# Performance work log

Measured on AMD Instinct MI355X. Metric: run time of the kernel, lower is better.

The kernel has to match this reference:

```python
import jax, jax.numpy as jnp
import numpy as np

NUM_TOURS = 200   # fixed segment count (original: tour_index.max()+1)
EPS = 1e-5        # torch InstanceNorm1d default eps


def setup_inputs() -> dict:
    key = jax.random.key(0)
    ks = jax.random.split(key, 9)
    B, P, D = 64, 2000, 128
    embeddings = jax.random.normal(ks[0], (B, P + 1, D), jnp.float32)
    tour_index = jax.random.randint(ks[1], (B, P), 0, NUM_TOURS, dtype=jnp.int32)
    # tour_combiner: Linear(2D -> D); feedforward: Linear(D -> D); stored as (in, out)
    W1 = jax.random.normal(ks[2], (2 * D, D), jnp.float32) / np.sqrt(2 * D)
    b1 = jax.random.normal(ks[3], (D,), jnp.float32) * 0.01
    W2 = jax.random.normal(ks[4], (D, D), jnp.float32) / np.sqrt(D)
    b2 = jax.random.normal(ks[5], (D,), jnp.float32) * 0.01
    # InstanceNorm1d affine params (per channel)
    gamma = 1.0 + 0.1 * jax.random.normal(ks[6], (D,), jnp.float32)
    beta = 0.1 * jax.random.normal(ks[7], (D,), jnp.float32)
    return {
        "batch_size": B, "num_customers": P,
        "tour_index": tour_index, "embeddings": embeddings,
        "W1": W1, "b1": b1, "W2": W2, "b2": b2,
        "gamma": gamma, "beta": beta,
    }


def reference(batch_size, num_customers, tour_index, embeddings, W1, b1, W2, b2, gamma, beta):
    B, P = batch_size, num_customers
    D = embeddings.shape[-1]
    cust = embeddings[:, 1:]                                  # (B, P, D)
    # tour-level segment sum (scatter_add over tour ids, per batch)
    flat_idx = (tour_index + jnp.arange(B, dtype=tour_index.dtype)[:, None] * NUM_TOURS).reshape(-1)
    tour_emb = jax.ops.segment_sum(cust.reshape(B * P, D), flat_idx,
                                   num_segments=B * NUM_TOURS).reshape(B, NUM_TOURS, D)
    # gather tour embedding back to each customer
    cust_tour = jnp.take_along_axis(tour_emb, tour_index[:, :, None], axis=1)  # (B, P, D)
    # concat -> linear -> relu -> linear
    combined = jnp.concatenate([cust, cust_tour], axis=-1)    # (B, P, 2D)
    h = jax.nn.relu(combined @ W1 + b1)
    h = h @ W2 + b2
    # residual + instance norm over the customer axis, per channel
    added = cust + h
    mean = jnp.mean(added, axis=1, keepdims=True)
    var = jnp.var(added, axis=1, keepdims=True)
    normed = (added - mean) * jax.lax.rsqrt(var + EPS) * gamma + beta
    return jnp.concatenate([embeddings[:, :1], normed], axis=1)
```

## Files before the change

kernel.cpp:

```cpp
#include <hip/hip_runtime.h>
#include <stdint.h>

typedef unsigned short u16;
typedef __attribute__((ext_vector_type(8))) short short8;
typedef __attribute__((ext_vector_type(4))) float floatx4;

constexpr int B_ = 64, P_ = 2000, D_ = 128, T_ = 200;

__device__ __forceinline__ u16 f2bf(float f) {
  union { float f; uint32_t u; } v; v.f = f;
  return (u16)((v.u + 0x7fffu + ((v.u >> 16) & 1u)) >> 16);
}

__global__ void k_zero(float* __restrict__ p, int n) {
  int i = blockIdx.x * 256 + threadIdx.x;
  if (i < n) p[i] = 0.f;
}

__global__ void k_prep_w(const float* __restrict__ W1, const float* __restrict__ W2,
                         u16* __restrict__ w1f, u16* __restrict__ w2f) {
  int tid = blockIdx.x * 256 + threadIdx.x;
  if (tid >= 6144) return;
  const float* W = (tid < 4096) ? W1 : W2;
  u16* dst = (tid < 4096) ? w1f : w2f;
  int fid = (tid < 4096) ? tid : tid - 4096;
  int lane = fid & 63;
  int nt = (fid >> 6) & 7;
  int ks = fid >> 9;
  int quad = lane >> 4, c = lane & 15;
  int k0 = ks * 32 + quad * 8;
#pragma unroll
  for (int j = 0; j < 8; ++j)
    dst[(size_t)fid * 8 + j] = f2bf(W[(k0 + j) * D_ + nt * 16 + c]);
}

__global__ __launch_bounds__(256) void k_bin(const int* __restrict__ tidx,
                                             int* __restrict__ list,
                                             int* __restrict__ goff,
                                             int* __restrict__ gcnt) {
  __shared__ int tix[P_];
  __shared__ int cnt[256], scan[256], cur[256];
  const int b = blockIdx.x, tid = threadIdx.x;
  cnt[tid] = 0;
  for (int i = tid; i < P_; i += 256) tix[i] = tidx[b * P_ + i];
  __syncthreads();
  for (int i = tid; i < P_; i += 256) atomicAdd(&cnt[tix[i]], 1);
  __syncthreads();
  scan[tid] = cnt[tid];
  __syncthreads();
  for (int s = 1; s < 256; s <<= 1) {
    int v = (tid >= s) ? scan[tid - s] : 0;
    __syncthreads();
    scan[tid] += v;
    __syncthreads();
  }
  int excl = scan[tid] - cnt[tid];
  if (tid < T_) {
    goff[b * T_ + tid] = excl;
    gcnt[b * T_ + tid] = cnt[tid];
  }
  cur[tid] = excl;
  __syncthreads();
  for (int i = tid; i < P_; i += 256) {
    int slot = atomicAdd(&cur[tix[i]], 1);
    list[b * P_ + slot] = i;
  }
}

__global__ __launch_bounds__(256) void k_gather(const float* __restrict__ emb,
                                                const int* __restrict__ list,
                                                const int* __restrict__ goff,
                                                const int* __restrict__ gcnt,
                                                u16* __restrict__ tourb) {
  const int tid = threadIdx.x;
  const int lane = tid & 63, wv = tid >> 6;
  const int seg = blockIdx.x * 4 + wv;
  const int b = seg / T_;
  const int off = goff[seg], cn = gcnt[seg];
  const int* lstb = list + b * P_;
  const float* eb = emb + ((size_t)(b * 2001 + 1)) * D_ + lane * 2;
  float sx = 0.f, sy = 0.f;
  for (int i = 0; i < cn; i += 8) {
    int pr[8];
#pragma unroll
    for (int j = 0; j < 8; ++j)
      if (i + j < cn) pr[j] = lstb[off + i + j];
    float2 v[8];
#pragma unroll
    for (int j = 0; j < 8; ++j)
      if (i + j < cn) v[j] = *(const float2*)(eb + (size_t)pr[j] * D_);
#pragma unroll
    for (int j = 0; j < 8; ++j)
      if (i + j < cn) { sx += v[j].x; sy += v[j].y; }
  }
  uint32_t pk = (uint32_t)f2bf(sx) | ((uint32_t)f2bf(sy) << 16);
  ((uint32_t*)(tourb + (size_t)seg * D_))[lane] = pk;
}

__global__ __launch_bounds__(256) void k_mlp(
    const int* __restrict__ tidx, const float* __restrict__ emb,
    const u16* __restrict__ tourb,
    const u16* __restrict__ w1f, const u16* __restrict__ w2f,
    const float* __restrict__ b1, const float* __restrict__ b2,
    float* __restrict__ out) {
  __shared__ u16 hbuf[128 * 136];
  const int tid = threadIdx.x;
  const int w = tid >> 6, lane = tid & 63, quad = lane >> 4, c = lane & 15;
  const int base = blockIdx.x * 128;
  const int r0 = w * 32;

  const float* arow[2];
  const u16* trow[2];
#pragma unroll
  for (int mt = 0; mt < 2; ++mt) {
    int m = base + r0 + mt * 16 + c;
    int b = m / P_, p = m - b * P_;
    arow[mt] = emb + ((size_t)(b * 2001 + 1 + p)) * D_;
    int t = tidx[m];
    trow[mt] = tourb + ((size_t)(b * T_ + t)) * D_;
  }
  float bias1[8], bias2[8];
#pragma unroll
  for (int nt = 0; nt < 8; ++nt) {
    bias1[nt] = b1[nt * 16 + c];
    bias2[nt] = b2[nt * 16 + c];
  }

  floatx4 acc[2][8];
#pragma unroll
  for (int mt = 0; mt < 2; ++mt)
#pragma unroll
    for (int nt = 0; nt < 8; ++nt) acc[mt][nt] = (floatx4)0.f;

#pragma unroll
  for (int ks = 0; ks < 8; ++ks) {
    short8 a[2];
#pragma unroll
    for (int mt = 0; mt < 2; ++mt) {
      if (ks < 4) {
        const float* src = arow[mt] + ks * 32 + quad * 8;
        floatx4 x0 = *(const floatx4*)src;
        floatx4 x1 = *(const floatx4*)(src + 4);
#pragma unroll
        for (int j = 0; j < 4; ++j) {
          a[mt][j]     = (short)f2bf(x0[j]);
          a[mt][4 + j] = (short)f2bf(x1[j]);
        }
      } else {
        a[mt] = *(const short8*)(trow[mt] + (ks - 4) * 32 + quad * 8);
      }
    }
#pragma unroll
    for (int nt = 0; nt < 8; ++nt) {
      short8 bf = *(const short8*)(w1f + ((size_t)((ks * 8 + nt) * 64 + lane)) * 8);
      acc[0][nt] = __builtin_amdgcn_mfma_f32_16x16x32_bf16(a[0], bf, acc[0][nt], 0, 0, 0);
      acc[1][nt] = __builtin_amdgcn_mfma_f32_16x16x32_bf16(a[1], bf, acc[1][nt], 0, 0, 0);
    }
  }

#pragma unroll
  for (int mt = 0; mt < 2; ++mt)
#pragma unroll
    for (int nt = 0; nt < 8; ++nt)
#pragma unroll
      for (int r = 0; r < 4; ++r) {
        int row = r0 + mt * 16 + quad * 4 + r;
        float v = acc[mt][nt][r] + bias1[nt];
        hbuf[row * 136 + nt * 16 + c] = f2bf(v > 0.f ? v : 0.f);
      }
  __syncthreads();

  floatx4 acc2[2][8];
#pragma unroll
  for (int mt = 0; mt < 2; ++mt)
#pragma unroll
    for (int nt = 0; nt < 8; ++nt) acc2[mt][nt] = (floatx4)0.f;

#pragma unroll
  for (int ks = 0; ks < 4; ++ks) {
    short8 a[2];
#pragma unroll
    for (int mt = 0; mt < 2; ++mt)
      a[mt] = *(const short8*)(&hbuf[(r0 + mt * 16 + c) * 136 + ks * 32 + quad * 8]);
#pragma unroll
    for (int nt = 0; nt < 8; ++nt) {
      short8 bf = *(const short8*)(w2f + ((size_t)((ks * 8 + nt) * 64 + lane)) * 8);
      acc2[0][nt] = __builtin_amdgcn_mfma_f32_16x16x32_bf16(a[0], bf, acc2[0][nt], 0, 0, 0);
      acc2[1][nt] = __builtin_amdgcn_mfma_f32_16x16x32_bf16(a[1], bf, acc2[1][nt], 0, 0, 0);
    }
  }

#pragma unroll
  for (int mt = 0; mt < 2; ++mt)
#pragma unroll
    for (int nt = 0; nt < 8; ++nt)
#pragma unroll
      for (int r = 0; r < 4; ++r) {
        int row = r0 + mt * 16 + quad * 4 + r;
        int m = base + row;
        int b = m / P_, p = m - b * P_;
        size_t gaddr = ((size_t)(b * 2001 + 1 + p)) * D_ + nt * 16 + c;
        out[gaddr] = emb[gaddr] + (acc2[mt][nt][r] + bias2[nt]);
      }
}

__global__ __launch_bounds__(256) void k_stats(const float* __restrict__ out,
                                               float* __restrict__ ssum,
                                               float* __restrict__ ssq) {
  const int b = blockIdx.y, ps = blockIdx.x;
  const int tid = threadIdx.x;
  const int col = tid & 127, rh = tid >> 7;
  float s = 0.f, s2 = 0.f;
  const float* src = out + ((size_t)b * 2001 + 1) * D_ + col;
  for (int p = ps * 125 + rh; p < ps * 125 + 125; p += 2) {
    float v = src[(size_t)p * D_];
    s += v; s2 += v * v;
  }
  __shared__ float ls[128], ls2[128];
  if (rh == 0) { ls[col] = s; ls2[col] = s2; }
  __syncthreads();
  if (rh == 1) { ls[col] += s; ls2[col] += s2; }
  __syncthreads();
  if (rh == 0) {
    atomicAdd(&ssum[b * D_ + col], ls[col]);
    atomicAdd(&ssq[b * D_ + col], ls2[col]);
  }
}

__global__ void k_final(const float* __restrict__ ssum, const float* __restrict__ ssq,
                        const float* __restrict__ gamma, const float* __restrict__ beta,
                        float* __restrict__ scale, float* __restrict__ shift) {
  int i = blockIdx.x * 256 + threadIdx.x;
  if (i >= B_ * D_) return;
  int col = i & 127;
  float mean = ssum[i] * (1.f / P_);
  float var = ssq[i] * (1.f / P_) - mean * mean;
  float rstd = rsqrtf(var + 1e-5f);
  float sc = rstd * gamma[col];
  scale[i] = sc;
  shift[i] = beta[col] - mean * sc;
}

__global__ __launch_bounds__(256) void k_out(
    const float* __restrict__ emb,
    const float* __restrict__ scale, const float* __restrict__ shift,
    float* __restrict__ out) {
  size_t i = ((size_t)blockIdx.x * 256 + threadIdx.x) * 8;
  int row = (int)(i >> 7), col = (int)(i & 127);
  int b = row / 2001, r = row - b * 2001;
  if (r == 0) {
    *(floatx4*)(out + i)     = *(const floatx4*)(emb + i);
    *(floatx4*)(out + i + 4) = *(const floatx4*)(emb + i + 4);
  } else {
    floatx4 a0 = *(const floatx4*)(out + i);
    floatx4 a1 = *(const floatx4*)(out + i + 4);
    int cc = b * D_ + col;
#pragma unroll
    for (int j = 0; j < 4; ++j) {
      a0[j] = a0[j] * scale[cc + j] + shift[cc + j];
      a1[j] = a1[j] * scale[cc + 4 + j] + shift[cc + 4 + j];
    }
    *(floatx4*)(out + i)     = a0;
    *(floatx4*)(out + i + 4) = a1;
  }
}

extern "C" void kernel_launch(void* const* d_in, const int* in_sizes, int n_in,
                              void* d_out, int out_size, void* d_ws, size_t ws_size,
                              hipStream_t stream) {
  const int*   tour_index = (const int*)d_in[2];
  const float* emb   = (const float*)d_in[3];
  const float* W1    = (const float*)d_in[4];
  const float* b1    = (const float*)d_in[5];
  const float* W2    = (const float*)d_in[6];
  const float* b2    = (const float*)d_in[7];
  const float* gamma = (const float*)d_in[8];
  const float* beta  = (const float*)d_in[9];
  float* out = (float*)d_out;
  char* ws = (char*)d_ws;

  u16*   w1f   = (u16*)(ws);
  u16*   w2f   = (u16*)(ws + 65536);
  float* ssum  = (float*)(ws + 98304);
  float* ssq   = ssum + B_ * D_;
  float* scale = (float*)(ws + 163840);
  float* shift = scale + B_ * D_;
  u16*   tourb = (u16*)(ws + 229376);
  int*   list  = (int*)(ws + 3506176);
  int*   goff  = (int*)(ws + 4018176);
  int*   gcnt  = (int*)(ws + 4069376);

  hipLaunchKernelGGL(k_zero,   dim3(64),     dim3(256), 0, stream, ssum, 2 * B_ * D_);
  hipLaunchKernelGGL(k_prep_w, dim3(24),     dim3(256), 0, stream, W1, W2, w1f, w2f);
  hipLaunchKernelGGL(k_bin,    dim3(64),     dim3(256), 0, stream, tour_index, list, goff, gcnt);
  hipLaunchKernelGGL(k_gather, dim3(3200),   dim3(256), 0, stream, emb, list, goff, gcnt, tourb);
  hipLaunchKernelGGL(k_mlp,    dim3(1000),   dim3(256), 0, stream, tour_index, emb, tourb,
                     w1f, w2f, b1, b2, out);
  hipLaunchKernelGGL(k_stats,  dim3(16, 64), dim3(256), 0, stream, out, ssum, ssq);
  hipLaunchKernelGGL(k_final,  dim3(32),     dim3(256), 0, stream, ssum, ssq, gamma, beta,
                     scale, shift);
  hipLaunchKernelGGL(k_out,    dim3(8004),   dim3(256), 0, stream, emb, scale, shift, out);
}
```

Measured before the change: 224.2 us.

## Fuse instance-norm statistics into MLP epilogue and stage residual in bf16

Drops the separate stats kernel: the MLP epilogue now accumulates per-channel sum and sum of squares, reduces them across the wave with shuffles and across the block through shared memory, then atomically adds them per batch. The grid is re-indexed per batch with 16 tiles of 128 rows and the last partial tile clamped, which adds some idle work. When the workspace is large enough, the pre-norm residual goes to a bf16 scratch buffer instead of fp32 output, halving that round-trip traffic but introducing bf16 rounding before normalization. Statistics are still computed in fp32.

```diff
diff --git a/kernel.cpp b/kernel.cpp
--- a/kernel.cpp
+++ b/kernel.cpp
@@ -10,6 +10,9 @@
 __device__ __forceinline__ u16 f2bf(float f) {
   union { float f; uint32_t u; } v; v.f = f;
   return (u16)((v.u + 0x7fffu + ((v.u >> 16) & 1u)) >> 16);
+}
+__device__ __forceinline__ float bf2f(u16 u) {
+  union { uint32_t u; float f; } v; v.u = ((uint32_t)u) << 16; return v.f;
 }
 
 __global__ void k_zero(float* __restrict__ p, int n) {
@@ -97,26 +100,29 @@
   ((uint32_t*)(tourb + (size_t)seg * D_))[lane] = pk;
 }
 
+template <bool BF>
 __global__ __launch_bounds__(256) void k_mlp(
     const int* __restrict__ tidx, const float* __restrict__ emb,
     const u16* __restrict__ tourb,
     const u16* __restrict__ w1f, const u16* __restrict__ w2f,
     const float* __restrict__ b1, const float* __restrict__ b2,
-    float* __restrict__ out) {
+    float* __restrict__ ssum, float* __restrict__ ssq,
+    u16* __restrict__ addedb, float* __restrict__ out) {
   __shared__ u16 hbuf[128 * 136];
   const int tid = threadIdx.x;
   const int w = tid >> 6, lane = tid & 63, quad = lane >> 4, c = lane & 15;
-  const int base = blockIdx.x * 128;
+  const int b = blockIdx.y;
+  const int p0 = blockIdx.x * 128;
   const int r0 = w * 32;
 
   const float* arow[2];
   const u16* trow[2];
 #pragma unroll
   for (int mt = 0; mt < 2; ++mt) {
-    int m = base + r0 + mt * 16 + c;
-    int b = m / P_, p = m - b * P_;
-    arow[mt] = emb + ((size_t)(b * 2001 + 1 + p)) * D_;
-    int t = tidx[m];
+    int p = p0 + r0 + mt * 16 + c;
+    int pc = p < P_ ? p : P_ - 1;
+    arow[mt] = emb + ((size_t)(b * 2001 + 1 + pc)) * D_;
+    int t = tidx[b * P_ + pc];
     trow[mt] = tourb + ((size_t)(b * T_ + t)) * D_;
   }
   float bias1[8], bias2[8];
@@ -190,6 +196,9 @@
     }
   }
 
+  float cs[8], cq[8];
+#pragma unroll
+  for (int nt = 0; nt < 8; ++nt) { cs[nt] = 0.f; cq[nt] = 0.f; }
 #pragma unroll
   for (int mt = 0; mt < 2; ++mt)
 #pragma unroll
@@ -197,33 +206,43 @@
 #pragma unroll
       for (int r = 0; r < 4; ++r) {
         int row = r0 + mt * 16 + quad * 4 + r;
-        int m = base + row;
-        int b = m / P_, p = m - b * P_;
-        size_t gaddr = ((size_t)(b * 2001 + 1 + p)) * D_ + nt * 16 + c;
-        out[gaddr] = emb[gaddr] + (acc2[mt][nt][r] + bias2[nt]);
+        int p = p0 + row;
+        int pc = p < P_ ? p : P_ - 1;
+        size_t gaddr = ((size_t)(b * 2001 + 1 + pc)) * D_ + nt * 16 + c;
+        float add = emb[gaddr] + (acc2[mt][nt][r] + bias2[nt]);
+        if (p < P_) {
+          if (BF) addedb[((size_t)(b * P_ + p)) * D_ + nt * 16 + c] = f2bf(add);
+          else    out[gaddr] = add;
+          cs[nt] += add;
+          cq[nt] += add * add;
+        }
       }
-}
-
-__global__ __launch_bounds__(256) void k_stats(const float* __restrict__ out,
-                                               float* __restrict__ ssum,
-                                               float* __restrict__ ssq) {
-  const int b = blockIdx.y, ps = blockIdx.x;
-  const int tid = threadIdx.x;
-  const int col = tid & 127, rh = tid >> 7;
-  float s = 0.f, s2 = 0.f;
-  const float* src = out + ((size_t)b * 2001 + 1) * D_ + col;
-  for (int p = ps * 125 + rh; p < ps * 125 + 125; p += 2) {
-    float v = src[(size_t)p * D_];
-    s += v; s2 += v * v;
-  }
-  __shared__ float ls[128], ls2[128];
-  if (rh == 0) { ls[col] = s; ls2[col] = s2; }
-  __syncthreads();
-  if (rh == 1) { ls[col] += s; ls2[col] += s2; }
-  __syncthreads();
-  if (rh == 0) {
-    atomicAdd(&ssum[b * D_ + col], ls[col]);
-    atomicAdd(&ssq[b * D_ + col], ls2[col]);
+#pragma unroll
+  for (int nt = 0; nt < 8; ++nt) {
+    cs[nt] += __shfl_xor(cs[nt], 16, 64);
+    cs[nt] += __shfl_xor(cs[nt], 32, 64);
+    cq[nt] += __shfl_xor(cq[nt], 16, 64);
+    cq[nt] += __shfl_xor(cq[nt], 32, 64);
+  }
+  float* sw = (float*)&hbuf[(size_t)r0 * 136];
+  if (quad == 0) {
+#pragma unroll
+    for (int nt = 0; nt < 8; ++nt) {
+      sw[nt * 16 + c] = cs[nt];
+      sw[128 + nt * 16 + c] = cq[nt];
+    }
+  }
+  __syncthreads();
+  if (tid < 128) {
+    float s = 0.f, q = 0.f;
+#pragma unroll
+    for (int wv = 0; wv < 4; ++wv) {
+      const float* sx = (const float*)&hbuf[(size_t)(wv * 32) * 136];
+      s += sx[tid];
+      q += sx[128 + tid];
+    }
+    atomicAdd(&ssum[b * D_ + tid], s);
+    atomicAdd(&ssq[b * D_ + tid], q);
   }
 }
 
@@ -241,8 +260,9 @@
   shift[i] = beta[col] - mean * sc;
 }
 
+template <bool BF>
 __global__ __launch_bounds__(256) void k_out(
-    const float* __restrict__ emb,
+    const float* __restrict__ emb, const u16* __restrict__ addedb,
     const float* __restrict__ scale, const float* __restrict__ shift,
     float* __restrict__ out) {
   size_t i = ((size_t)blockIdx.x * 256 + threadIdx.x) * 8;
@@ -252,9 +272,19 @@
     *(floatx4*)(out + i)     = *(const floatx4*)(emb + i);
     *(floatx4*)(out + i + 4) = *(const floatx4*)(emb + i + 4);
   } else {
-    floatx4 a0 = *(const floatx4*)(out + i);
-    floatx4 a1 = *(const floatx4*)(out + i + 4);
     int cc = b * D_ + col;
+    floatx4 a0, a1;
+    if (BF) {
+      short8 av = *(const short8*)(addedb + ((size_t)(b * P_ + r - 1)) * D_ + col);
+#pragma unroll
+      for (int j = 0; j < 4; ++j) {
+        a0[j] = bf2f((u16)av[j]);
+        a1[j] = bf2f((u16)av[4 + j]);
+      }
+    } else {
+      a0 = *(const floatx4*)(out + i);
+      a1 = *(const floatx4*)(out + i + 4);
+    }
 #pragma unroll
     for (int j = 0; j < 4; ++j) {
       a0[j] = a0[j] * scale[cc + j] + shift[cc + j];
@@ -289,15 +319,27 @@
   int*   list  = (int*)(ws + 3506176);
   int*   goff  = (int*)(ws + 4018176);
   int*   gcnt  = (int*)(ws + 4069376);
+  u16*   addedb = (u16*)(ws + 4120576);
+  const bool big = ws_size >= (size_t)4120576 + 32768000;
 
   hipLaunchKernelGGL(k_zero,   dim3(64),     dim3(256), 0, stream, ssum, 2 * B_ * D_);
   hipLaunchKernelGGL(k_prep_w, dim3(24),     dim3(256), 0, stream, W1, W2, w1f, w2f);
   hipLaunchKernelGGL(k_bin,    dim3(64),     dim3(256), 0, stream, tour_index, list, goff, gcnt);
   hipLaunchKernelGGL(k_gather, dim3(3200),   dim3(256), 0, stream, emb, list, goff, gcnt, tourb);
-  hipLaunchKernelGGL(k_mlp,    dim3(1000),   dim3(256), 0, stream, tour_index, emb, tourb,
-                     w1f, w2f, b1, b2, out);
-  hipLaunchKernelGGL(k_stats,  dim3(16, 64), dim3(256), 0, stream, out, ssum, ssq);
+  if (big) {
+    hipLaunchKernelGGL(HIP_KERNEL_NAME(k_mlp<true>), dim3(16, 64), dim3(256), 0, stream,
+                       tour_index, emb, tourb, w1f, w2f, b1, b2, ssum, ssq, addedb, out);
+  } else {
+    hipLaunchKernelGGL(HIP_KERNEL_NAME(k_mlp<false>), dim3(16, 64), dim3(256), 0, stream,
+                       tour_index, emb, tourb, w1f, w2f, b1, b2, ssum, ssq, addedb, out);
+  }
   hipLaunchKernelGGL(k_final,  dim3(32),     dim3(256), 0, stream, ssum, ssq, gamma, beta,
                      scale, shift);
-  hipLaunchKernelGGL(k_out,    dim3(8004),   dim3(256), 0, stream, emb, scale, shift, out);
-}
+  if (big) {
+    hipLaunchKernelGGL(HIP_KERNEL_NAME(k_out<true>),  dim3(8004), dim3(256), 0, stream,
+                       emb, addedb, scale, shift, out);
+  } else {
+    hipLaunchKernelGGL(HIP_KERNEL_NAME(k_out<false>), dim3(8004), dim3(256), 0, stream,
+                       emb, addedb, scale, shift, out);
+  }
+}
```

Result: no change. 225.5 us (+0.6%).
